# Optimization experiments

Hardware: AMD Instinct MI355X
Metric: run time of the kernel (lower is better)

Reference implementation:

```python
import jax, jax.numpy as jnp
import numpy as np

N_NODES = 50000


def _sage_gcn_layer(h, src, dst, W, b, n_nodes):
    # DGL SAGEConv with aggregator 'gcn':
    # h_neigh = (sum_{u in N(v)} h_u + h_v) / (in_deg(v) + 1); out = h_neigh @ W + b
    neigh = jax.ops.segment_sum(h[src], dst, num_segments=n_nodes)  # [N, d]
    deg = jax.ops.segment_sum(jnp.ones((src.shape[0],), h.dtype), dst,
                              num_segments=n_nodes)  # in-degree [N]
    h_agg = (neigh + h) / (deg[:, None] + 1.0)
    return h_agg @ W + b


def setup_inputs() -> dict:
    key = jax.random.key(0)
    ks = jax.random.split(key, 8)
    in_f, hid, out_c, E = 128, 16, 16, 800000
    x = jax.random.normal(ks[0], (N_NODES, in_f), jnp.float32)
    src = jax.random.randint(ks[1], (E,), 0, N_NODES)
    dst = jax.random.randint(ks[2], (E,), 0, N_NODES)
    W1 = jax.random.normal(ks[3], (in_f, hid), jnp.float32) * (1.0 / np.sqrt(in_f))
    b1 = jnp.zeros((hid,), jnp.float32)
    W2 = jax.random.normal(ks[4], (hid, in_f), jnp.float32) * (1.0 / np.sqrt(hid))
    b2 = jnp.zeros((in_f,), jnp.float32)
    Wmlp = jax.random.normal(ks[5], (2 * in_f, out_c), jnp.float32) * (1.0 / np.sqrt(2 * in_f))
    bmlp = jnp.zeros((out_c,), jnp.float32)
    return {"x": x, "src": src, "dst": dst, "W1": W1, "b1": b1,
            "W2": W2, "b2": b2, "Wmlp": Wmlp, "bmlp": bmlp}


def reference(x, src, dst, W1, b1, W2, b2, Wmlp, bmlp):
    n = x.shape[0]
    # SAGE (dropout is identity in eval mode)
    h = _sage_gcn_layer(x, src, dst, W1, b1, n)          # [N, 16]
    h = jax.nn.relu(h)
    h = _sage_gcn_layer(h, src, dst, W2, b2, n)          # [N, in_f]
    # MLPPredictor: per-edge gather-concat-linear
    h_u = h[src]                                         # [E, in_f]
    h_v = h[dst]                                         # [E, in_f]
    score = jnp.concatenate([h_u, h_v], axis=1) @ Wmlp + bmlp  # [E, out_c]
    return score
```

## Files before the change

kernel.cpp:

```cpp
#include <hip/hip_runtime.h>

#define IN_F 128
#define HID  16

#define NBKT 256
#define RANGE 196
#define BKT_CAP 4096
#define P1_EDGES 4096

__global__ void precompute_kernel(const float* __restrict__ W2,
                                  const float* __restrict__ b2,
                                  const float* __restrict__ Wmlp,
                                  const float* __restrict__ bmlp,
                                  float* __restrict__ CA,
                                  float* __restrict__ CB,
                                  float* __restrict__ cbias) {
    int t = threadIdx.x;
    int j = t >> 4, c = t & 15;
    float sa = 0.f, sb = 0.f;
    for (int k = 0; k < 128; ++k) {
        float w = W2[j * 128 + k];
        sa += w * Wmlp[k * 16 + c];
        sb += w * Wmlp[(128 + k) * 16 + c];
    }
    CA[j * 16 + c] = sa;
    CB[j * 16 + c] = sb;
    if (j == 0) {
        float s = bmlp[c];
        for (int k = 0; k < 128; ++k)
            s += b2[k] * (Wmlp[k * 16 + c] + Wmlp[(128 + k) * 16 + c]);
        cbias[c] = s;
    }
}

__global__ void xw1_kernel(const float* __restrict__ x,
                           const float* __restrict__ W1,
                           float* __restrict__ y, int N) {
    __shared__ float W1s[128 * 16];
    __shared__ float xs[16][128];
    int tid = threadIdx.x;
    const float4* W14 = (const float4*)W1;
    float4* W1s4 = (float4*)W1s;
    for (int i = tid; i < 512; i += 256) W1s4[i] = W14[i];
    int nblk = blockIdx.x * 16;
    const float4* x4 = (const float4*)x;
    float4* xs4 = (float4*)&xs[0][0];
    for (int i = tid; i < 512; i += 256) {
        int row = nblk + (i >> 5);
        xs4[i] = (row < N) ? x4[(size_t)row * 32 + (i & 31)]
                           : make_float4(0.f, 0.f, 0.f, 0.f);
    }
    __syncthreads();
    int nl = tid >> 4, j = tid & 15;
    int n = nblk + nl;
    if (n >= N) return;
    float acc = 0.f;
    const float* xr = &xs[nl][0];
    #pragma unroll 8
    for (int k = 0; k < 128; ++k) acc += xr[k] * W1s[k * 16 + j];
    y[(size_t)n * 16 + j] = acc;
}

__global__ void __launch_bounds__(1024)
bucket_bin_kernel(const int* __restrict__ src, const int* __restrict__ dst,
                  int* __restrict__ bc,
                  int* __restrict__ bdst,
                  int* __restrict__ bsrc,
                  int E) {
    __shared__ int hist[NBKT], lstart[NBKT], lcur[NBKT], gbase[NBKT];
    __shared__ int sd[P1_EDGES], ss[P1_EDGES];
    int tid = threadIdx.x;
    if (tid < NBKT) { hist[tid] = 0; lcur[tid] = 0; }
    __syncthreads();

    int base = blockIdx.x * P1_EDGES + tid * 4;
    int d[4], s[4], cnt = 0;
    if (base + 3 < E) {
        int4 dd = *(const int4*)(dst + base);
        int4 sv = *(const int4*)(src + base);
        d[0] = dd.x; d[1] = dd.y; d[2] = dd.z; d[3] = dd.w;
        s[0] = sv.x; s[1] = sv.y; s[2] = sv.z; s[3] = sv.w;
        cnt = 4;
    } else {
        for (int e = base; e < E; ++e) { d[cnt] = dst[e]; s[cnt] = src[e]; ++cnt; }
    }
    for (int i = 0; i < cnt; ++i) atomicAdd(&hist[d[i] / RANGE], 1);
    __syncthreads();

    int v = (tid < NBKT) ? hist[tid] : 0;
    if (tid < NBKT) lstart[tid] = v;
    __syncthreads();
    for (int off = 1; off < NBKT; off <<= 1) {
        int t = 0;
        if (tid < NBKT && tid >= off) t = lstart[tid - off];
        __syncthreads();
        if (tid < NBKT) lstart[tid] += t;
        __syncthreads();
    }
    if (tid < NBKT) {
        lstart[tid] -= v;
        gbase[tid] = tid * BKT_CAP + atomicAdd(&bc[tid], v);
    }
    __syncthreads();

    for (int i = 0; i < cnt; ++i) {
        int b = d[i] / RANGE;
        int r = atomicAdd(&lcur[b], 1);
        int p = lstart[b] + r;
        sd[p] = d[i]; ss[p] = s[i];
    }
    __syncthreads();

    int tot = lstart[NBKT - 1] + hist[NBKT - 1];
    for (int i = tid; i < tot; i += 1024) {
        int dv = sd[i];
        int b = dv / RANGE;
        int g = gbase[b] + (i - lstart[b]);
        bdst[g] = dv;
        bsrc[g] = ss[i];
    }
}

__global__ void count_kernel(const int* __restrict__ bc,
                             const int* __restrict__ bdst,
                             int* __restrict__ count, int N) {
    __shared__ int cnt[RANGE];
    int b = blockIdx.x, tid = threadIdx.x;
    if (tid < RANGE) cnt[tid] = 0;
    __syncthreads();
    int m = bc[b], base_node = b * RANGE;
    const int* bp = bdst + b * BKT_CAP;
    for (int i = tid; i < m; i += 256) atomicAdd(&cnt[bp[i] - base_node], 1);
    __syncthreads();
    if (tid < RANGE && base_node + tid < N) count[base_node + tid] = cnt[tid];
}

__global__ void scan_partial_kernel(const int* __restrict__ count,
                                    int* __restrict__ psum, int N) {
    __shared__ int s[256];
    int i = blockIdx.x * 256 + threadIdx.x;
    s[threadIdx.x] = (i < N) ? count[i] : 0;
    __syncthreads();
    for (int off = 128; off > 0; off >>= 1) {
        if (threadIdx.x < off) s[threadIdx.x] += s[threadIdx.x + off];
        __syncthreads();
    }
    if (threadIdx.x == 0) psum[blockIdx.x] = s[0];
}

__global__ void scan_top_kernel(int* __restrict__ psum, int nb) {
    __shared__ int s[1024];
    int v = (threadIdx.x < nb) ? psum[threadIdx.x] : 0;
    s[threadIdx.x] = v;
    __syncthreads();
    for (int off = 1; off < 1024; off <<= 1) {
        int t = (threadIdx.x >= off) ? s[threadIdx.x - off] : 0;
        __syncthreads();
        s[threadIdx.x] += t;
        __syncthreads();
    }
    if (threadIdx.x < nb) psum[threadIdx.x] = s[threadIdx.x] - v;
}

__global__ void scan_final_kernel(const int* __restrict__ count,
                                  const int* __restrict__ psum,
                                  int* __restrict__ row_ptr, int N, int E) {
    __shared__ int s[256];
    int i = blockIdx.x * 256 + threadIdx.x;
    int v = (i < N) ? count[i] : 0;
    s[threadIdx.x] = v;
    __syncthreads();
    for (int off = 1; off < 256; off <<= 1) {
        int t = (threadIdx.x >= off) ? s[threadIdx.x - off] : 0;
        __syncthreads();
        s[threadIdx.x] += t;
        __syncthreads();
    }
    if (i < N) row_ptr[i] = psum[blockIdx.x] + s[threadIdx.x] - v;
    if (i == N - 1) row_ptr[N] = E;
}

__global__ void bucket_scatter_kernel(const int* __restrict__ bc,
                                      const int* __restrict__ bdst,
                                      const int* __restrict__ bsrc,
                                      const int* __restrict__ row_ptr,
                                      int* __restrict__ sorted_src, int N) {
    __shared__ int lcur[RANGE];
    __shared__ int stage[BKT_CAP];
    int b = blockIdx.x, tid = threadIdx.x;
    int base_node = b * RANGE;
    int rbase = row_ptr[base_node];
    if (tid < RANGE) {
        int nn = base_node + tid;
        lcur[tid] = (nn < N) ? row_ptr[nn] - rbase : 0;
    }
    __syncthreads();
    int m = bc[b];
    const int* bd = bdst + b * BKT_CAP;
    const int* bs = bsrc + b * BKT_CAP;
    for (int i = tid; i < m; i += 256) {
        int n = bd[i] - base_node;
        int p = atomicAdd(&lcur[n], 1);
        stage[p] = bs[i];
    }
    __syncthreads();
    for (int i = tid; i < m; i += 256) sorted_src[rbase + i] = stage[i];
}

__global__ void agg1_kernel(const int* __restrict__ row_ptr,
                            const int* __restrict__ sorted_src,
                            const float4* __restrict__ y4,
                            const float* __restrict__ b1,
                            float4* __restrict__ h14,
                            float* __restrict__ invdeg, int N) {
    int lane = threadIdx.x & 63, wid = threadIdx.x >> 6;
    int n = blockIdx.x * 4 + wid;
    if (n >= N) return;
    int q = lane & 3, kk = lane >> 2;
    int beg = row_ptr[n], end = row_ptr[n + 1];
    float4 acc = make_float4(0.f, 0.f, 0.f, 0.f);
    if (kk == 0) acc = y4[(size_t)n * 4 + q];
    for (int k = beg + kk; k < end; k += 16) {
        int s = sorted_src[k];
        float4 v = y4[(size_t)s * 4 + q];
        acc.x += v.x; acc.y += v.y; acc.z += v.z; acc.w += v.w;
    }
    #pragma unroll
    for (int off = 4; off < 64; off <<= 1) {
        acc.x += __shfl_xor(acc.x, off);
        acc.y += __shfl_xor(acc.y, off);
        acc.z += __shfl_xor(acc.z, off);
        acc.w += __shfl_xor(acc.w, off);
    }
    if (kk == 0) {
        float inv = 1.0f / (float)(end - beg + 1);
        float4 b = ((const float4*)b1)[q];
        float4 r;
        r.x = fmaxf(fmaf(acc.x, inv, b.x), 0.f);
        r.y = fmaxf(fmaf(acc.y, inv, b.y), 0.f);
        r.z = fmaxf(fmaf(acc.z, inv, b.z), 0.f);
        r.w = fmaxf(fmaf(acc.w, inv, b.w), 0.f);
        h14[(size_t)n * 4 + q] = r;
        if (q == 0) invdeg[n] = inv;
    }
}

__global__ void agg2_kernel(const int* __restrict__ row_ptr,
                            const int* __restrict__ sorted_src,
                            const float4* __restrict__ h14,
                            const float* __restrict__ invdeg,
                            const float* __restrict__ CA,
                            const float* __restrict__ CB,
                            float* __restrict__ su,
                            float* __restrict__ sv, int N) {
    __shared__ float CAs[256], CBs[256];
    __shared__ float gs[4][16];
    int tid = threadIdx.x;
    CAs[tid] = CA[tid];
    CBs[tid] = CB[tid];
    int lane = tid & 63, wid = tid >> 6;
    int n = blockIdx.x * 4 + wid;
    int q = lane & 3, kk = lane >> 2;
    if (n < N) {
        int beg = row_ptr[n], end = row_ptr[n + 1];
        float4 acc = make_float4(0.f, 0.f, 0.f, 0.f);
        if (kk == 0) acc = h14[(size_t)n * 4 + q];
        for (int k = beg + kk; k < end; k += 16) {
            int s = sorted_src[k];
            float4 v = h14[(size_t)s * 4 + q];
            acc.x += v.x; acc.y += v.y; acc.z += v.z; acc.w += v.w;
        }
        #pragma unroll
        for (int off = 4; off < 64; off <<= 1) {
            acc.x += __shfl_xor(acc.x, off);
            acc.y += __shfl_xor(acc.y, off);
            acc.z += __shfl_xor(acc.z, off);
            acc.w += __shfl_xor(acc.w, off);
        }
        if (kk == 0) {
            float inv = invdeg[n];
            ((float4*)gs[wid])[q] =
                make_float4(acc.x * inv, acc.y * inv, acc.z * inv, acc.w * inv);
        }
    }
    __syncthreads();
    if (lane < 32 && n < N) {
        int c = lane & 15, sel = lane >> 4;
        const float* C = sel ? CBs : CAs;
        float sum = 0.f;
        #pragma unroll
        for (int j = 0; j < 16; ++j) sum += gs[wid][j] * C[j * 16 + c];
        float* dp = sel ? sv : su;
        dp[(size_t)n * 16 + c] = sum;
    }
}

__global__ void score_kernel(const int* __restrict__ src,
                             const int* __restrict__ dst,
                             const float4* __restrict__ su4,
                             const float4* __restrict__ sv4,
                             const float* __restrict__ cbias,
                             float4* __restrict__ out4, int E) {
    int e = blockIdx.x * 256 + threadIdx.x;
    if (e >= E) return;
    int s = src[e], d = dst[e];
    const float4* cb4 = (const float4*)cbias;
    #pragma unroll
    for (int q = 0; q < 4; ++q) {
        float4 a = su4[(size_t)s * 4 + q];
        float4 b = sv4[(size_t)d * 4 + q];
        float4 cb = cb4[q];
        float4 r;
        r.x = a.x + b.x + cb.x;
        r.y = a.y + b.y + cb.y;
        r.z = a.z + b.z + cb.z;
        r.w = a.w + b.w + cb.w;
        out4[(size_t)e * 4 + q] = r;
    }
}

extern "C" void kernel_launch(void* const* d_in, const int* in_sizes, int n_in,
                              void* d_out, int out_size, void* d_ws, size_t ws_size,
                              hipStream_t stream) {
    const float* x    = (const float*)d_in[0];
    const int*   src  = (const int*)  d_in[1];
    const int*   dst  = (const int*)  d_in[2];
    const float* W1   = (const float*)d_in[3];
    const float* b1   = (const float*)d_in[4];
    const float* W2   = (const float*)d_in[5];
    const float* b2   = (const float*)d_in[6];
    const float* Wmlp = (const float*)d_in[7];
    const float* bmlp = (const float*)d_in[8];
    float* out = (float*)d_out;

    const int N = in_sizes[0] / IN_F;
    const int E = in_sizes[1];
    const int nb = (N + 255) / 256;

    int* bc         = (int*)d_ws;
    int* bdst       = bc + NBKT;
    int* bsrc       = bdst + NBKT * BKT_CAP;
    int* sorted_src = bsrc + NBKT * BKT_CAP;
    int* count      = sorted_src + E;
    int* psum       = count + N;
    int* row_ptr    = psum + 1024;
    size_t intcnt = (size_t)NBKT + 2 * (size_t)NBKT * BKT_CAP + (size_t)E +
                    (size_t)N + 1024 + (size_t)(N + 1);
    intcnt = (intcnt + 3) & ~(size_t)3;
    float* y      = (float*)d_ws + intcnt;
    float* h1     = y + (size_t)N * 16;
    float* su     = h1 + (size_t)N * 16;
    float* sv     = su + (size_t)N * 16;
    float* invdeg = sv + (size_t)N * 16;
    float* CA     = invdeg + N;
    float* CB     = CA + 256;
    float* cbias  = CB + 256;

    hipMemsetAsync(bc, 0, NBKT * sizeof(int), stream);

    const int p1Blocks   = (E + P1_EDGES - 1) / P1_EDGES;
    const int edgeBlocks = (E + 255) / 256;
    const int nodeBlocks16 = (N + 15) / 16;
    const int nodeBlocks4  = (N + 3) / 4;

    precompute_kernel<<<1, 256, 0, stream>>>(W2, b2, Wmlp, bmlp, CA, CB, cbias);
    xw1_kernel<<<nodeBlocks16, 256, 0, stream>>>(x, W1, y, N);
    bucket_bin_kernel<<<p1Blocks, 1024, 0, stream>>>(src, dst, bc, bdst, bsrc, E);
    count_kernel<<<NBKT, 256, 0, stream>>>(bc, bdst, count, N);
    scan_partial_kernel<<<nb, 256, 0, stream>>>(count, psum, N);
    scan_top_kernel<<<1, 1024, 0, stream>>>(psum, nb);
    scan_final_kernel<<<nb, 256, 0, stream>>>(count, psum, row_ptr, N, E);
    bucket_scatter_kernel<<<NBKT, 256, 0, stream>>>(bc, bdst, bsrc, row_ptr,
                                                    sorted_src, N);
    agg1_kernel<<<nodeBlocks4, 256, 0, stream>>>(row_ptr, sorted_src,
                                                 (const float4*)y, b1,
                                                 (float4*)h1, invdeg, N);
    agg2_kernel<<<nodeBlocks4, 256, 0, stream>>>(row_ptr, sorted_src,
                                                 (const float4*)h1, invdeg,
                                                 CA, CB, su, sv, N);
    score_kernel<<<edgeBlocks, 256, 0, stream>>>(src, dst, (const float4*)su,
                                                 (const float4*)sv, cbias,
                                                 (float4*)out, E);
}
```

Measured before the change: 225.5 us.

## Aggregate directly from dst buckets with shared-memory atomics, dropping CSR build

Removes the count, three-stage scan and bucket scatter kernels that built a CSR row_ptr/sorted_src. Both aggregation layers now run one 1024-thread block per destination bucket, gather source features and accumulate them into a shared-memory per-node accumulator with float atomics, counting degree the same way. This cuts five launches and the global traffic of sorting, in exchange for shared-memory atomic contention, only 256 blocks of parallelism, and order-dependent float summation.

```diff
diff --git a/kernel.cpp b/kernel.cpp
--- a/kernel.cpp
+++ b/kernel.cpp
@@ -121,177 +121,106 @@
     }
 }
 
-__global__ void count_kernel(const int* __restrict__ bc,
-                             const int* __restrict__ bdst,
-                             int* __restrict__ count, int N) {
-    __shared__ int cnt[RANGE];
-    int b = blockIdx.x, tid = threadIdx.x;
-    if (tid < RANGE) cnt[tid] = 0;
-    __syncthreads();
+__global__ void __launch_bounds__(1024)
+agg1b_kernel(const int* __restrict__ bc,
+             const int* __restrict__ bdst,
+             const int* __restrict__ bsrc,
+             const float4* __restrict__ y4,
+             const float* __restrict__ b1,
+             const float* __restrict__ y,
+             float* __restrict__ h1,
+             float* __restrict__ invdeg, int N) {
+    __shared__ float acc[RANGE][17];
+    __shared__ int degc[RANGE];
+    int tid = threadIdx.x;
+    for (int i = tid; i < RANGE * 17; i += 1024) (&acc[0][0])[i] = 0.f;
+    if (tid < RANGE) degc[tid] = 0;
+    __syncthreads();
+
+    int b = blockIdx.x;
     int m = bc[b], base_node = b * RANGE;
-    const int* bp = bdst + b * BKT_CAP;
-    for (int i = tid; i < m; i += 256) atomicAdd(&cnt[bp[i] - base_node], 1);
-    __syncthreads();
-    if (tid < RANGE && base_node + tid < N) count[base_node + tid] = cnt[tid];
-}
-
-__global__ void scan_partial_kernel(const int* __restrict__ count,
-                                    int* __restrict__ psum, int N) {
-    __shared__ int s[256];
-    int i = blockIdx.x * 256 + threadIdx.x;
-    s[threadIdx.x] = (i < N) ? count[i] : 0;
-    __syncthreads();
-    for (int off = 128; off > 0; off >>= 1) {
-        if (threadIdx.x < off) s[threadIdx.x] += s[threadIdx.x + off];
-        __syncthreads();
-    }
-    if (threadIdx.x == 0) psum[blockIdx.x] = s[0];
-}
-
-__global__ void scan_top_kernel(int* __restrict__ psum, int nb) {
-    __shared__ int s[1024];
-    int v = (threadIdx.x < nb) ? psum[threadIdx.x] : 0;
-    s[threadIdx.x] = v;
-    __syncthreads();
-    for (int off = 1; off < 1024; off <<= 1) {
-        int t = (threadIdx.x >= off) ? s[threadIdx.x - off] : 0;
-        __syncthreads();
-        s[threadIdx.x] += t;
-        __syncthreads();
-    }
-    if (threadIdx.x < nb) psum[threadIdx.x] = s[threadIdx.x] - v;
-}
-
-__global__ void scan_final_kernel(const int* __restrict__ count,
-                                  const int* __restrict__ psum,
-                                  int* __restrict__ row_ptr, int N, int E) {
-    __shared__ int s[256];
-    int i = blockIdx.x * 256 + threadIdx.x;
-    int v = (i < N) ? count[i] : 0;
-    s[threadIdx.x] = v;
-    __syncthreads();
-    for (int off = 1; off < 256; off <<= 1) {
-        int t = (threadIdx.x >= off) ? s[threadIdx.x - off] : 0;
-        __syncthreads();
-        s[threadIdx.x] += t;
-        __syncthreads();
-    }
-    if (i < N) row_ptr[i] = psum[blockIdx.x] + s[threadIdx.x] - v;
-    if (i == N - 1) row_ptr[N] = E;
-}
-
-__global__ void bucket_scatter_kernel(const int* __restrict__ bc,
-                                      const int* __restrict__ bdst,
-                                      const int* __restrict__ bsrc,
-                                      const int* __restrict__ row_ptr,
-                                      int* __restrict__ sorted_src, int N) {
-    __shared__ int lcur[RANGE];
-    __shared__ int stage[BKT_CAP];
-    int b = blockIdx.x, tid = threadIdx.x;
-    int base_node = b * RANGE;
-    int rbase = row_ptr[base_node];
-    if (tid < RANGE) {
-        int nn = base_node + tid;
-        lcur[tid] = (nn < N) ? row_ptr[nn] - rbase : 0;
-    }
-    __syncthreads();
-    int m = bc[b];
     const int* bd = bdst + b * BKT_CAP;
     const int* bs = bsrc + b * BKT_CAP;
-    for (int i = tid; i < m; i += 256) {
-        int n = bd[i] - base_node;
-        int p = atomicAdd(&lcur[n], 1);
-        stage[p] = bs[i];
-    }
-    __syncthreads();
-    for (int i = tid; i < m; i += 256) sorted_src[rbase + i] = stage[i];
-}
-
-__global__ void agg1_kernel(const int* __restrict__ row_ptr,
-                            const int* __restrict__ sorted_src,
-                            const float4* __restrict__ y4,
-                            const float* __restrict__ b1,
-                            float4* __restrict__ h14,
-                            float* __restrict__ invdeg, int N) {
-    int lane = threadIdx.x & 63, wid = threadIdx.x >> 6;
-    int n = blockIdx.x * 4 + wid;
-    if (n >= N) return;
-    int q = lane & 3, kk = lane >> 2;
-    int beg = row_ptr[n], end = row_ptr[n + 1];
-    float4 acc = make_float4(0.f, 0.f, 0.f, 0.f);
-    if (kk == 0) acc = y4[(size_t)n * 4 + q];
-    for (int k = beg + kk; k < end; k += 16) {
-        int s = sorted_src[k];
+    int slot = tid >> 2, q = tid & 3;
+    for (int k = slot; k < m; k += 256) {
+        int n = bd[k] - base_node;
+        int s = bs[k];
         float4 v = y4[(size_t)s * 4 + q];
-        acc.x += v.x; acc.y += v.y; acc.z += v.z; acc.w += v.w;
-    }
-    #pragma unroll
-    for (int off = 4; off < 64; off <<= 1) {
-        acc.x += __shfl_xor(acc.x, off);
-        acc.y += __shfl_xor(acc.y, off);
-        acc.z += __shfl_xor(acc.z, off);
-        acc.w += __shfl_xor(acc.w, off);
-    }
-    if (kk == 0) {
-        float inv = 1.0f / (float)(end - beg + 1);
-        float4 b = ((const float4*)b1)[q];
-        float4 r;
-        r.x = fmaxf(fmaf(acc.x, inv, b.x), 0.f);
-        r.y = fmaxf(fmaf(acc.y, inv, b.y), 0.f);
-        r.z = fmaxf(fmaf(acc.z, inv, b.z), 0.f);
-        r.w = fmaxf(fmaf(acc.w, inv, b.w), 0.f);
-        h14[(size_t)n * 4 + q] = r;
-        if (q == 0) invdeg[n] = inv;
-    }
-}
-
-__global__ void agg2_kernel(const int* __restrict__ row_ptr,
-                            const int* __restrict__ sorted_src,
-                            const float4* __restrict__ h14,
-                            const float* __restrict__ invdeg,
-                            const float* __restrict__ CA,
-                            const float* __restrict__ CB,
-                            float* __restrict__ su,
-                            float* __restrict__ sv, int N) {
+        atomicAdd(&acc[n][q * 4 + 0], v.x);
+        atomicAdd(&acc[n][q * 4 + 1], v.y);
+        atomicAdd(&acc[n][q * 4 + 2], v.z);
+        atomicAdd(&acc[n][q * 4 + 3], v.w);
+        if (q == 0) atomicAdd(&degc[n], 1);
+    }
+    __syncthreads();
+
+    for (int i = tid; i < RANGE * 16; i += 1024) {
+        int n = i >> 4, c = i & 15;
+        int node = base_node + n;
+        if (node >= N) continue;
+        float inv = 1.0f / (float)(degc[n] + 1);
+        float val = fmaf(acc[n][c] + y[(size_t)node * 16 + c], inv, b1[c]);
+        h1[(size_t)node * 16 + c] = val > 0.f ? val : 0.f;
+        if (c == 0) invdeg[node] = inv;
+    }
+}
+
+__global__ void __launch_bounds__(1024)
+agg2b_kernel(const int* __restrict__ bc,
+             const int* __restrict__ bdst,
+             const int* __restrict__ bsrc,
+             const float4* __restrict__ h14,
+             const float* __restrict__ h1,
+             const float* __restrict__ invdeg,
+             const float* __restrict__ CA,
+             const float* __restrict__ CB,
+             float* __restrict__ su,
+             float* __restrict__ sv, int N) {
+    __shared__ float acc[RANGE][17];
+    __shared__ float g[RANGE][17];
     __shared__ float CAs[256], CBs[256];
-    __shared__ float gs[4][16];
-    int tid = threadIdx.x;
-    CAs[tid] = CA[tid];
-    CBs[tid] = CB[tid];
-    int lane = tid & 63, wid = tid >> 6;
-    int n = blockIdx.x * 4 + wid;
-    int q = lane & 3, kk = lane >> 2;
-    if (n < N) {
-        int beg = row_ptr[n], end = row_ptr[n + 1];
-        float4 acc = make_float4(0.f, 0.f, 0.f, 0.f);
-        if (kk == 0) acc = h14[(size_t)n * 4 + q];
-        for (int k = beg + kk; k < end; k += 16) {
-            int s = sorted_src[k];
-            float4 v = h14[(size_t)s * 4 + q];
-            acc.x += v.x; acc.y += v.y; acc.z += v.z; acc.w += v.w;
+    int tid = threadIdx.x;
+    for (int i = tid; i < RANGE * 17; i += 1024) (&acc[0][0])[i] = 0.f;
+    if (tid < 256) { CAs[tid] = CA[tid]; CBs[tid] = CB[tid]; }
+    __syncthreads();
+
+    int b = blockIdx.x;
+    int m = bc[b], base_node = b * RANGE;
+    const int* bd = bdst + b * BKT_CAP;
+    const int* bs = bsrc + b * BKT_CAP;
+    int slot = tid >> 2, q = tid & 3;
+    for (int k = slot; k < m; k += 256) {
+        int n = bd[k] - base_node;
+        int s = bs[k];
+        float4 v = h14[(size_t)s * 4 + q];
+        atomicAdd(&acc[n][q * 4 + 0], v.x);
+        atomicAdd(&acc[n][q * 4 + 1], v.y);
+        atomicAdd(&acc[n][q * 4 + 2], v.z);
+        atomicAdd(&acc[n][q * 4 + 3], v.w);
+    }
+    __syncthreads();
+
+    for (int i = tid; i < RANGE * 16; i += 1024) {
+        int n = i >> 4, c = i & 15;
+        int node = base_node + n;
+        g[n][c] = (node < N)
+            ? (acc[n][c] + h1[(size_t)node * 16 + c]) * invdeg[node] : 0.f;
+    }
+    __syncthreads();
+
+    for (int i = tid; i < RANGE * 16; i += 1024) {
+        int n = i >> 4, c = i & 15;
+        int node = base_node + n;
+        if (node >= N) continue;
+        float sa = 0.f, sb = 0.f;
+        #pragma unroll
+        for (int j = 0; j < 16; ++j) {
+            float gj = g[n][j];
+            sa += gj * CAs[j * 16 + c];
+            sb += gj * CBs[j * 16 + c];
         }
-        #pragma unroll
-        for (int off = 4; off < 64; off <<= 1) {
-            acc.x += __shfl_xor(acc.x, off);
-            acc.y += __shfl_xor(acc.y, off);
-            acc.z += __shfl_xor(acc.z, off);
-            acc.w += __shfl_xor(acc.w, off);
-        }
-        if (kk == 0) {
-            float inv = invdeg[n];
-            ((float4*)gs[wid])[q] =
-                make_float4(acc.x * inv, acc.y * inv, acc.z * inv, acc.w * inv);
-        }
-    }
-    __syncthreads();
-    if (lane < 32 && n < N) {
-        int c = lane & 15, sel = lane >> 4;
-        const float* C = sel ? CBs : CAs;
-        float sum = 0.f;
-        #pragma unroll
-        for (int j = 0; j < 16; ++j) sum += gs[wid][j] * C[j * 16 + c];
-        float* dp = sel ? sv : su;
-        dp[(size_t)n * 16 + c] = sum;
+        su[(size_t)node * 16 + c] = sa;
+        sv[(size_t)node * 16 + c] = sb;
     }
 }
 
@@ -335,18 +264,11 @@
 
     const int N = in_sizes[0] / IN_F;
     const int E = in_sizes[1];
-    const int nb = (N + 255) / 256;
-
-    int* bc         = (int*)d_ws;
-    int* bdst       = bc + NBKT;
-    int* bsrc       = bdst + NBKT * BKT_CAP;
-    int* sorted_src = bsrc + NBKT * BKT_CAP;
-    int* count      = sorted_src + E;
-    int* psum       = count + N;
-    int* row_ptr    = psum + 1024;
-    size_t intcnt = (size_t)NBKT + 2 * (size_t)NBKT * BKT_CAP + (size_t)E +
-                    (size_t)N + 1024 + (size_t)(N + 1);
-    intcnt = (intcnt + 3) & ~(size_t)3;
+
+    int* bc   = (int*)d_ws;
+    int* bdst = bc + NBKT;
+    int* bsrc = bdst + NBKT * BKT_CAP;
+    size_t intcnt = (size_t)NBKT + 2 * (size_t)NBKT * BKT_CAP;
     float* y      = (float*)d_ws + intcnt;
     float* h1     = y + (size_t)N * 16;
     float* su     = h1 + (size_t)N * 16;
@@ -358,26 +280,17 @@
 
     hipMemsetAsync(bc, 0, NBKT * sizeof(int), stream);
 
-    const int p1Blocks   = (E + P1_EDGES - 1) / P1_EDGES;
-    const int edgeBlocks = (E + 255) / 256;
+    const int p1Blocks     = (E + P1_EDGES - 1) / P1_EDGES;
+    const int edgeBlocks   = (E + 255) / 256;
     const int nodeBlocks16 = (N + 15) / 16;
-    const int nodeBlocks4  = (N + 3) / 4;
 
     precompute_kernel<<<1, 256, 0, stream>>>(W2, b2, Wmlp, bmlp, CA, CB, cbias);
     xw1_kernel<<<nodeBlocks16, 256, 0, stream>>>(x, W1, y, N);
     bucket_bin_kernel<<<p1Blocks, 1024, 0, stream>>>(src, dst, bc, bdst, bsrc, E);
-    count_kernel<<<NBKT, 256, 0, stream>>>(bc, bdst, count, N);
-    scan_partial_kernel<<<nb, 256, 0, stream>>>(count, psum, N);
-    scan_top_kernel<<<1, 1024, 0, stream>>>(psum, nb);
-    scan_final_kernel<<<nb, 256, 0, stream>>>(count, psum, row_ptr, N, E);
-    bucket_scatter_kernel<<<NBKT, 256, 0, stream>>>(bc, bdst, bsrc, row_ptr,
-                                                    sorted_src, N);
-    agg1_kernel<<<nodeBlocks4, 256, 0, stream>>>(row_ptr, sorted_src,
-                                                 (const float4*)y, b1,
-                                                 (float4*)h1, invdeg, N);
-    agg2_kernel<<<nodeBlocks4, 256, 0, stream>>>(row_ptr, sorted_src,
-                                                 (const float4*)h1, invdeg,
-                                                 CA, CB, su, sv, N);
+    agg1b_kernel<<<NBKT, 1024, 0, stream>>>(bc, bdst, bsrc, (const float4*)y,
+                                            b1, y, h1, invdeg, N);
+    agg2b_kernel<<<NBKT, 1024, 0, stream>>>(bc, bdst, bsrc, (const float4*)h1,
+                                            h1, invdeg, CA, CB, su, sv, N);
     score_kernel<<<edgeBlocks, 256, 0, stream>>>(src, dst, (const float4*)su,
                                                  (const float4*)sv, cbias,
                                                  (float4*)out, E);
```

Result: slower. 302.7 us (+34.2%).
